# Optimization experiments

Hardware: AMD Instinct MI355X
Metric: run time of the kernel (lower is better)

The kernel has to match this reference:

```python
import jax, jax.numpy as jnp
import numpy as np

B, S, D_MODEL, D_HEAD = 8, 2048, 1024, 128
MAX_ROUNDS = 3
THRESH = 0.1
SCALE = 1.0 / np.sqrt(float(D_HEAD))


def setup_inputs() -> dict:
    key = jax.random.key(0)
    ks = jax.random.split(key, 12)

    def lin(k, out_d, in_d):
        # torch Linear weight layout [out, in], y = x @ W.T + b
        return (jax.random.normal(k, (out_d, in_d), jnp.float32) / np.sqrt(float(in_d))).astype(jnp.float32)

    thesis_w = lin(ks[3], D_HEAD, D_HEAD)
    return {
        "x": jax.random.normal(ks[0], (B, S, D_MODEL), jnp.float32),
        "wq": lin(ks[1], D_HEAD, D_MODEL),
        "wk": lin(ks[2], D_HEAD, D_MODEL),
        "wv": lin(ks[4], D_HEAD, D_MODEL),
        "thesis_w": thesis_w,  # antithesis weight is -thesis_w per __init__
        "thesis_b": 0.02 * jax.random.normal(ks[5], (D_HEAD,), jnp.float32),
        "anti_b": 0.02 * jax.random.normal(ks[6], (D_HEAD,), jnp.float32),
        "s_w1": lin(ks[7], D_HEAD, 3 * D_HEAD),
        "s_b1": jnp.zeros((D_HEAD,), jnp.float32),
        "s_w2": lin(ks[8], D_HEAD, D_HEAD),
        "s_b2": jnp.zeros((D_HEAD,), jnp.float32),
        "g_w": lin(ks[9], 1, 2 * D_HEAD),
        "g_b": jnp.zeros((1,), jnp.float32),
    }


def reference(x, wq, wk, wv, thesis_w, thesis_b, anti_b, s_w1, s_b1, s_w2, s_b2, g_w, g_b):
    # q/k/v projections (no bias)
    q = jnp.einsum("bsm,hm->bsh", x, wq)
    k = jnp.einsum("bsm,hm->bsh", x, wk)
    v = jnp.einsum("bsm,hm->bsh", x, wv)

    attn = jax.nn.softmax(jnp.einsum("bqh,bkh->bqk", q, k) * SCALE, axis=-1)
    # dropout is identity at eval time
    cur = jnp.einsum("bqk,bkh->bqh", attn, v)  # [B,S,Dh]

    # attn_weights and v never change across rounds, so thesis/antithesis are
    # round-invariant: compute the context projections once.
    context = cur
    thesis = context @ thesis_w.T + thesis_b
    anti = context @ (-thesis_w).T + anti_b  # antithesis weight = -thesis weight

    active = jnp.ones((B, S), dtype=bool)
    for _ in range(MAX_ROUNDS):
        # emulate `if not active_mask.any(): break` under jit
        any_active = jnp.any(active)
        am = active[..., None].astype(x.dtype)
        at, aa, ac = thesis * am, anti * am, cur * am

        h = jax.nn.relu(jnp.concatenate([at, aa, ac], axis=-1) @ s_w1.T + s_b1)
        synth = h @ s_w2.T + s_b2
        gate = jax.nn.sigmoid(jnp.concatenate([ac, synth], axis=-1) @ g_w.T + g_b)
        update = gate * (synth - ac) * 0.1
        new = cur + update  # applied to ALL tokens, matching original

        stable = jnp.linalg.norm(update, axis=-1) < THRESH  # new - cur == update
        cur = jnp.where(any_active, new, cur)
        active = jnp.where(any_active, active & ~stable, active)
    return cur
```

## Files before the change

### kernel.cpp

```cpp
#include <hip/hip_runtime.h>
#include <hip/hip_bf16.h>

#define B_   8
#define S_   2048
#define DM   1024
#define DH   128
#define BS_  16384
#define SCALE_  0.08838834764831845f
#define SCALE2_ 0.12751744f

typedef unsigned short u16;
typedef unsigned int   u32;
typedef _Float16 half8 __attribute__((ext_vector_type(8)));
typedef __bf16   bf16x8 __attribute__((ext_vector_type(8)));
typedef float    f32x4 __attribute__((ext_vector_type(4)));
typedef u32      u32x4 __attribute__((ext_vector_type(4)));

union H8 { u32x4 v; u32 u[4]; half8 h; bf16x8 b; };

__device__ __forceinline__ float bf2f(u16 u) {
    union { u32 i; float f; } w; w.i = ((u32)u) << 16; return w.f;
}
__device__ __forceinline__ void unpack8(uint4 v, float* f) {
    f[0] = bf2f(v.x & 0xffff); f[1] = bf2f(v.x >> 16);
// ... 208 lines not shown
                u32 w[4];
#pragma unroll
                for (int q = 0; q < 4; ++q)
                    w[q] = (u32)TS[key][d0 + 2 * q] | ((u32)TS[key][d0 + 2 * q + 1] << 16);
                kfrag[((size_t)(m0 / 16 + sub) * 4 + ks) * 64 + lf] = (u32x4){w[0], w[1], w[2], w[3]};
            }
        } else {
#pragma unroll
            for (int i = 0; i < 4; ++i) {
                const int f = tid + 256 * i;
                const int lf = f & 63, t = (f >> 6) & 7, sub = f >> 9;
                const int kb2 = sub * 32 + 8 * (lf >> 4);
                const int dh  = 16 * t + (lf & 15);
                u32 w[4];
#pragma unroll
                for (int q = 0; q < 4; ++q)
                    w[q] = (u32)TS[kb2 + 2 * q][dh] | ((u32)TS[kb2 + 2 * q + 1][dh] << 16);
                vfrag[((size_t)(m0 / 32 + sub) * 8 + t) * 64 + lf] = (u32x4){w[0], w[1], w[2], w[3]};
            }
        }
    }
}

template <bool WRITE_PARTIAL>
__device__ __forceinline__ void attn_body(
    const u32* qp, const u32x4* __restrict__ kfrag, const u32x4* __restrict__ vfrag,
    u16* outO, u16* outL, float* cur,
    int b, int q0, int kt0, int kt1, int part)
{
    const int tid = threadIdx.x;
    const int wave = tid >> 6, lane = tid & 63;
    const int qd = lane >> 4, c = lane & 15;

    __shared__ __align__(16) u16 PB[4][640];

    H8 Qh[4];
    {
        const u32* qr = qp + ((size_t)b * S_ + q0 + wave * 16 + c) * DH;
#pragma unroll
        for (int ks = 0; ks < 4; ++ks) {
            uint4 e0 = *(const uint4*)(qr + ks * 32 + qd * 8);
            uint4 e1 = *(const uint4*)(qr + ks * 32 + qd * 8 + 4);
            Qh[ks].u[0] = permHI(e0.y, e0.x); Qh[ks].u[1] = permHI(e0.w, e0.z);
            Qh[ks].u[2] = permHI(e1.y, e1.x); Qh[ks].u[3] = permHI(e1.w, e1.z);
        }
    }

    f32x4 O[8] = {};
    float lsum[4] = {};

    const u32x4* kb0 = kfrag + (size_t)b * 128 * 256;
    const u32x4* vb0 = vfrag + (size_t)b * 64 * 512;

    for (int kt = kt0; kt < kt1; ++kt) {
        const u32x4* kf = kb0 + (size_t)kt * 512;
        const u32x4* vf = vb0 + (size_t)kt * 512;

        f32x4 S0 = {}, S1 = {};
        __builtin_amdgcn_s_setprio(1);
#pragma unroll
        for (int ks = 0; ks < 4; ++ks) {
            H8 kh;
            kh.v = kf[ks * 64 + lane];
            S0 = __builtin_amdgcn_mfma_f32_16x16x32_f16(Qh[ks].h, kh.h, S0, 0, 0, 0);
            kh.v = kf[256 + ks * 64 + lane];
            S1 = __builtin_amdgcn_mfma_f32_16x16x32_f16(Qh[ks].h, kh.h, S1, 0, 0, 0);
        }
        __builtin_amdgcn_s_setprio(0);

        u16* pw = PB[wave];
#pragma unroll
        for (int r = 0; r < 4; ++r) {
            float e0 = exp2f(fmaf(S0[r], SCALE2_, -4.0f));
            float e1 = exp2f(fmaf(S1[r], SCALE2_, -4.0f));
            lsum[r] += e0 + e1;
            pw[(4 * qd + r) * 40 + c]      = f2h(e0);
            pw[(4 * qd + r) * 40 + 16 + c] = f2h(e1);
        }

        uint4 ev = *(const uint4*)&pw[c * 40 + 8 * qd];
        H8 Ph;
        Ph.u[0] = ev.x; Ph.u[1] = ev.y; Ph.u[2] = ev.z; Ph.u[3] = ev.w;

        __builtin_amdgcn_s_setprio(1);
#pragma unroll
        for (int t = 0; t < 8; ++t) {
            H8 vh;
            vh.v = vf[t * 64 + lane];
            O[t] = __builtin_amdgcn_mfma_f32_16x16x32_f16(Ph.h, vh.h, O[t], 0, 0, 0);
        }
        __builtin_amdgcn_s_setprio(0);
    }

    if (WRITE_PARTIAL) {
        float lred[4];
#pragma unroll
        for (int r = 0; r < 4; ++r) {
            float l = lsum[r];
            l += __shfl_xor(l, 1); l += __shfl_xor(l, 2);
            l += __shfl_xor(l, 4); l += __shfl_xor(l, 8);
            lred[r] = l;
        }
        const size_t rb = (size_t)b * S_ + q0 + wave * 16 + 4 * qd;
        u16* Op = outO + (size_t)part * ((size_t)BS_ * DH);
#pragma unroll
        for (int t = 0; t < 8; ++t)
#pragma unroll
            for (int r = 0; r < 4; ++r)
                Op[(rb + r) * DH + t * 16 + c] = f2h(O[t][r]);
        if (c == 0) {
            u16* lp = outL + (size_t)part * BS_;
#pragma unroll
            for (int r = 0; r < 4; ++r) lp[rb + r] = f2h(lred[r]);
        }
    } else {
        float linv[4];
#pragma unroll
        for (int r = 0; r < 4; ++r) {
            float l = lsum[r];
            l += __shfl_xor(l, 1); l += __shfl_xor(l, 2);
            l += __shfl_xor(l, 4); l += __shfl_xor(l, 8);
            linv[r] = 1.0f / l;
        }
        const size_t rb = (size_t)b * S_ + q0 + wave * 16 + 4 * qd;
#pragma unroll
        for (int t = 0; t < 8; ++t)
#pragma unroll
            for (int r = 0; r < 4; ++r)
                cur[(rb + r) * DH + t * 16 + c] = O[t][r] * linv[r];
    }
}

__global__ __launch_bounds__(256) void attn_kernel(
    const u32* qp, const u32x4* __restrict__ kfrag, const u32x4* __restrict__ vfrag, float* cur)
{
    const int rid = blockIdx.x + 32 * blockIdx.y;
    attn_body<false>(qp, kfrag, vfrag, nullptr, nullptr, cur,
                     rid & 7, ((rid >> 3) & 31) * 64, 0, S_ / 32, 0);
}

__global__ __launch_bounds__(256) void attn_split_kernel(
    const u32* qp, const u32x4* __restrict__ kfrag, const u32x4* __restrict__ vfrag,
    u16* __restrict__ Opart, u16* __restrict__ lpart)
{
    const int rid = blockIdx.x + 32 * (blockIdx.y + 8 * blockIdx.z);
    const int b    = rid & 7;
    const int qx   = (rid >> 3) & 31;
    const int part = rid >> 8;
    const int quart = S_ / 128;
    attn_body<true>(qp, kfrag, vfrag, Opart, lpart, nullptr,
                    b, qx * 64, part * quart, (part + 1) * quart, part);
}

__global__ __launch_bounds__(256) void combine_kernel(
    const u16* __restrict__ Opart, const u16* __restrict__ lpart,
    float* __restrict__ cur)
{
    const size_t N1 = (size_t)BS_ * DH;
    const size_t i0 = ((size_t)blockIdx.x * 256 + threadIdx.x) * 16;
    const int row = (int)(i0 >> 7);
    const float lt = h2f(lpart[row]) + h2f(lpart[BS_ + row])
                   + h2f(lpart[2 * BS_ + row]) + h2f(lpart[3 * BS_ + row]);
    const float linv = 1.0f / lt;
    float acc[16] = {};
#pragma unroll
    for (int p = 0; p < 4; ++p) {
        const u16* op = Opart + (size_t)p * N1 + i0;
        uint4 v0 = *(const uint4*)op;
        uint4 v1 = *(const uint4*)(op + 8);
        const u32 w[8] = {v0.x, v0.y, v0.z, v0.w, v1.x, v1.y, v1.z, v1.w};
#pragma unroll
        for (int j = 0; j < 8; ++j) {
            acc[2 * j]     += h2f((u16)(w[j] & 0xffff));
            acc[2 * j + 1] += h2f((u16)(w[j] >> 16));
        }
    }
#pragma unroll
    for (int t = 0; t < 4; ++t)
        *(float4*)(cur + i0 + t * 4) = make_float4(
            acc[4*t] * linv, acc[4*t+1] * linv, acc[4*t+2] * linv, acc[4*t+3] * linv);
}

__global__ __launch_bounds__(256) void prepack_rw_kernel(
    const void* __restrict__ tw, const void* __restrict__ w1, const void* __restrict__ w2,
    const int* __restrict__ flag, u32x4* __restrict__ pk)
{
    const int isb = *flag;
    const int gid = blockIdx.x * 256 + threadIdx.x;
    const int l = gid & 63, t = (gid >> 6) & 7, ks = (gid >> 9) & 3, mat = gid >> 11;
    const int row = 16 * t + (l & 15);
    const int k0  = ks * 32 + 8 * (l >> 4);
    float f[8];
    if (mat == 0)      ld8(tw, (size_t)row * DH + k0, isb, f);
    else if (mat <= 3) ld8(w1, (size_t)row * 384 + (mat - 1) * 128 + k0, isb, f);
    else               ld8(w2, (size_t)row * DH + k0, isb, f);
    u32x4 hi, lo;
    split8(f, hi, lo);
    const size_t base = (((size_t)mat * 4 + ks) * 16 + 2 * t) * 64 + l;
    pk[base] = hi; pk[base + 64] = lo;
}

struct Afrag { H8 h[4], l[4]; };
__device__ __forceinline__ void splitA(const float (&A)[4][8], Afrag& F) {
#pragma unroll
    for (int ks = 0; ks < 4; ++ks) split8(A[ks], F.h[ks].v, F.l[ks].v);
}

__global__ __launch_bounds__(256) void round_kernel(
    const float* cur0, const float* curr,
    const u32x4* __restrict__ pk, u16* __restrict__ T0,
    const void* __restrict__ tb, const void* __restrict__ ab,
    const void* __restrict__ b1, const void* __restrict__ b2,
    const void* __restrict__ gw, const void* __restrict__ gb,
    const int* __restrict__ flag, int* active, int* counts, int r,
    float* cur_out, void* dout)
{
    const int isb = *flag;
    const int tok0 = blockIdx.x * 16;
    const int tid = threadIdx.x;
    const bool last = (dout != nullptr);

    if (counts[r] <= 0) {
        if (last) {
            for (int e = tid; e < 16 * DH; e += 256) {
                size_t idx = (size_t)tok0 * DH + e;
                float v = curr[idx];
                if (isb) ((__hip_bfloat16*)dout)[idx] = __float2bfloat16(v);
                else     ((float*)dout)[idx] = v;
            }
        }
        return;
    }

    const int wave = tid >> 6, lane = tid & 63;
    const int qd = lane >> 4, c = lane & 15;

    __shared__ u32x4 WB[2][2][8][64];
    __shared__ u16 TS[16][132];
    __shared__ float actS[16], tbS[128], abS[128], b1S[128], b2S[128], gwS[256];
    __shared__ int blkcnt;

    auto stageBh = [&](int mat, int h) {
#pragma unroll
        for (int j = 0; j < 4; ++j) {
            const int g = wave * 4 + j, kl = g >> 3, t = g & 7;
            __builtin_amdgcn_global_load_lds(
                (const __attribute__((address_space(1))) u32*)(
                    pk + (((size_t)mat * 4 + 2 * h + kl) * 16 + 2 * t) * 64 + lane),
                (__attribute__((address_space(3))) u32*)&WB[h][kl][t][0],
                16, 0, 0);
        }
    };
    auto gemmBh = [&](const Afrag& F, int h, f32x4 (&acc)[2]) {
#pragma unroll
        for (int kl = 0; kl < 2; ++kl) {
            const int ks = 2 * h + kl;
#pragma unroll
            for (int tl = 0; tl < 2; ++tl) {
                H8 bh; bh.v = WB[h][kl][2 * wave + tl][lane];
                acc[tl] = __builtin_amdgcn_mfma_f32_16x16x32_f16(F.l[ks].h, bh.h, acc[tl], 0, 0, 0);
                acc[tl] = __builtin_amdgcn_mfma_f32_16x16x32_f16(F.h[ks].h, bh.h, acc[tl], 0, 0, 0);
            }
        }
    };
    auto stageFq = [&](int mat, int q, int buf) {
#pragma unroll
        for (int j = 0; j < 4; ++j) {
            const int g = wave * 4 + j, p = g & 1, t = g >> 1;
            __builtin_amdgcn_global_load_lds(
                (const __attribute__((address_space(1))) u32*)(
                    pk + (((size_t)mat * 4 + q) * 16 + 2 * t + p) * 64 + lane),
                (__attribute__((address_space(3))) u32*)&WB[buf][p][t][0],
                16, 0, 0);
        }
    };
    auto gemmFq = [&](const Afrag& F, int q, int buf, f32x4 (&acc)[2]) {
#pragma unroll
        for (int tl = 0; tl < 2; ++tl) {
            H8 bh, bl;
            bh.v = WB[buf][0][2 * wave + tl][lane];
            bl.v = WB[buf][1][2 * wave + tl][lane];
            acc[tl] = __builtin_amdgcn_mfma_f32_16x16x32_f16(F.l[q].h, bh.h, acc[tl], 0, 0, 0);
            acc[tl] = __builtin_amdgcn_mfma_f32_16x16x32_f16(F.h[q].h, bl.h, acc[tl], 0, 0, 0);
            acc[tl] = __builtin_amdgcn_mfma_f32_16x16x32_f16(F.h[q].h, bh.h, acc[tl], 0, 0, 0);
        }
    };
    auto GEMMF = [&](int mat, const Afrag& F, f32x4 (&acc)[2]) {
        for (int q = 0; q < 4; ++q) {
            stageFq(mat, q, q & 1);
            __syncthreads();
            gemmFq(F, q, q & 1, acc);
            __syncthreads();
        }
    };

    const int hr = 4 * qd;
    const int rowl = c;

    auto writeTS = [&](const f32x4 (&acc)[2], const float* bias, bool relu) {
#pragma unroll
        for (int tl = 0; tl < 2; ++tl)
#pragma unroll
            for (int rr = 0; rr < 4; ++rr) {
                const int col = 16 * (2 * wave + tl) + c;
                float v = acc[tl][rr] + (bias ? bias[col] : 0.0f);
                TS[hr + rr][col] = f2h(relu ? fmaxf(v, 0.0f) : v);
            }
    };
    auto buildAt = [&](Afrag& F, float am_r) {
        float Ac[4][8];
#pragma unroll
        for (int ks = 0; ks < 4; ++ks)
#pragma unroll
            for (int j = 0; j < 8; ++j) {
                const int k = ks * 32 + 8 * qd + j;
                Ac[ks][j] = (h2f(TS[rowl][k]) + tbS[k]) * am_r;
            }
        splitA(Ac, F);
    };
    auto buildAa = [&](Afrag& F, float am_r) {
        float Ac[4][8];
#pragma unroll
        for (int ks = 0; ks < 4; ++ks)
#pragma unroll
            for (int j = 0; j < 8; ++j) {
                const int k = ks * 32 + 8 * qd + j;
                Ac[ks][j] = (abS[k] - h2f(TS[rowl][k])) * am_r;
            }
        splitA(Ac, F);
    };
    auto buildAc = [&](Afrag& F, float am_r) {
        float Ac[4][8];
        const float* cr = curr + (size_t)(tok0 + rowl) * DH;
#pragma unroll
        for (int ks = 0; ks < 4; ++ks) {
            float4 a0 = *(const float4*)(cr + ks * 32 + 8 * qd);
            float4 a1 = *(const float4*)(cr + ks * 32 + 8 * qd + 4);
            Ac[ks][0] = a0.x * am_r; Ac[ks][1] = a0.y * am_r;
            Ac[ks][2] = a0.z * am_r; Ac[ks][3] = a0.w * am_r;
            Ac[ks][4] = a1.x * am_r; Ac[ks][5] = a1.y * am_r;
            Ac[ks][6] = a1.z * am_r; Ac[ks][7] = a1.w * am_r;
        }
        splitA(Ac, F);
    };
    auto buildAh = [&](Afrag& F) {
        float Ac[4][8];
#pragma unroll
        for (int ks = 0; ks < 4; ++ks)
#pragma unroll
            for (int j = 0; j < 8; ++j)
                Ac[ks][j] = h2f(TS[rowl][ks * 32 + 8 * qd + j]);
        splitA(Ac, F);
    };

    if (tid < 16) actS[tid] = active[tok0 + tid] ? 1.0f : 0.0f;
    if (tid < 128) {
        tbS[tid] = ldE(tb, tid, isb); abS[tid] = ldE(ab, tid, isb);
        b1S[tid] = ldE(b1, tid, isb); b2S[tid] = ldE(b2, tid, isb);
    }
    gwS[tid] = ldE(gw, tid, isb);
    if (tid == 0) blkcnt = 0;
    const float gbf = ldE(gb, 0, isb);

    if (isb) {
        f32x4 acc1[2] = {};
        if (r == 0) {
            float A1[4][8];
            const float* cr = cur0 + (size_t)(tok0 + rowl) * DH;
#pragma unroll
            for (int ks = 0; ks < 4; ++ks) {
                *(float4*)&A1[ks][0] = *(const float4*)(cr + ks * 32 + 8 * qd);
                *(float4*)&A1[ks][4] = *(const float4*)(cr + ks * 32 + 8 * qd + 4);
            }
            Afrag FA; splitA(A1, FA);
            stageBh(0, 0);
            __syncthreads();
            stageBh(0, 1);
            f32x4 accT[2] = {};
            gemmBh(FA, 0, accT);
            __syncthreads();
            stageBh(1, 0);
            gemmBh(FA, 1, accT);
            writeTS(accT, nullptr, false);
            __syncthreads();
            for (int i = tid; i < 16 * 64; i += 256) {
                const int row = i >> 6, c2 = (i & 63) * 2;
                *(u32*)&T0[(size_t)(tok0 + row) * DH + c2] = *(const u32*)&TS[row][c2];
            }
        } else {
            stageBh(1, 0);
            for (int i = tid; i < 16 * 64; i += 256) {
                const int row = i >> 6, c2 = (i & 63) * 2;
                *(u32*)&TS[row][c2] = *(const u32*)&T0[(size_t)(tok0 + row) * DH + c2];
            }
            __syncthreads();
        }
        const float am_r = actS[rowl];
        {
            Afrag FC; buildAt(FC, am_r);
            stageBh(1, 1);
            gemmBh(FC, 0, acc1);
            __syncthreads();
            stageBh(2, 0);
            gemmBh(FC, 1, acc1);
            __syncthreads();
        }
        {
            Afrag FC; buildAa(FC, am_r);
            stageBh(2, 1);
            gemmBh(FC, 0, acc1);
            __syncthreads();
            stageBh(3, 0);
            gemmBh(FC, 1, acc1);
            __syncthreads();
        }
        {
            Afrag FC; buildAc(FC, am_r);
            stageBh(3, 1);
            gemmBh(FC, 0, acc1);
            __syncthreads();
            stageBh(4, 0);
            gemmBh(FC, 1, acc1);
        }
        writeTS(acc1, b1S, true);
        __syncthreads();
        {
            Afrag FC; buildAh(FC);
            stageBh(4, 1);
            f32x4 acc2[2] = {};
            gemmBh(FC, 0, acc2);
            __syncthreads();
            gemmBh(FC, 1, acc2);
            writeTS(acc2, b2S, false);
        }
        __syncthreads();
    } else {
        __syncthreads();
        f32x4 acc1[2] = {};
        if (r == 0) {
            float A1[4][8];
            const float* cr = cur0 + (size_t)(tok0 + rowl) * DH;
#pragma unroll
            for (int ks = 0; ks < 4; ++ks) {
                *(float4*)&A1[ks][0] = *(const float4*)(cr + ks * 32 + 8 * qd);
                *(float4*)&A1[ks][4] = *(const float4*)(cr + ks * 32 + 8 * qd + 4);
            }
            Afrag FA; splitA(A1, FA);
            f32x4 accT[2] = {};
            GEMMF(0, FA, accT);
            writeTS(accT, nullptr, false);
            __syncthreads();
            for (int i = tid; i < 16 * 64; i += 256) {
                const int row = i >> 6, c2 = (i & 63) * 2;
                *(u32*)&T0[(size_t)(tok0 + row) * DH + c2] = *(const u32*)&TS[row][c2];
            }
        } else {
            for (int i = tid; i < 16 * 64; i += 256) {
                const int row = i >> 6, c2 = (i & 63) * 2;
                *(u32*)&TS[row][c2] = *(const u32*)&T0[(size_t)(tok0 + row) * DH + c2];
            }
            __syncthreads();
        }
        const float am_r = actS[rowl];
        { Afrag FC; buildAt(FC, am_r); GEMMF(1, FC, acc1); }
        { Afrag FC; buildAa(FC, am_r); GEMMF(2, FC, acc1); }
        { Afrag FC; buildAc(FC, am_r); GEMMF(3, FC, acc1); }
        writeTS(acc1, b1S, true);
        __syncthreads();
        {
            Afrag FC; buildAh(FC);
            f32x4 acc2[2] = {};
            GEMMF(4, FC, acc2);
            writeTS(acc2, b2S, false);
        }
        __syncthreads();
    }

    const int tok = tid >> 4, d0 = (tid & 15) * 8;
    const float am = actS[tok];
    const float* cp = curr + (size_t)(tok0 + tok) * DH + d0;
    float cv[8];
    {
        float4 v0 = *(const float4*)cp;
        float4 v1 = *(const float4*)(cp + 4);
        cv[0] = v0.x; cv[1] = v0.y; cv[2] = v0.z; cv[3] = v0.w;
        cv[4] = v1.x; cv[5] = v1.y; cv[6] = v1.z; cv[7] = v1.w;
    }
    float srow[8];
#pragma unroll
    for (int e = 0; e < 8; ++e) srow[e] = h2f(TS[tok][d0 + e]);
    float gp = 0.0f;
#pragma unroll
    for (int e = 0; e < 8; ++e)
        gp += cv[e] * am * gwS[d0 + e] + srow[e] * gwS[128 + d0 + e];
    gp += __shfl_xor(gp, 1, 16);
    gp += __shfl_xor(gp, 2, 16);
    gp += __shfl_xor(gp, 4, 16);
    gp += __shfl_xor(gp, 8, 16);
    const float gate = 1.0f / (1.0f + __expf(-(gp + gbf)));
    float ss = 0.0f; float up[8];
#pragma unroll
    for (int e = 0; e < 8; ++e) {
        float u = gate * (srow[e] - cv[e] * am) * 0.1f;
        up[e] = u; ss += u * u;
    }
    ss += __shfl_xor(ss, 1, 16);
    ss += __shfl_xor(ss, 2, 16);
    ss += __shfl_xor(ss, 4, 16);
    ss += __shfl_xor(ss, 8, 16);
    const bool stable = sqrtf(ss) < 0.1f;

    if (last) {
        size_t off = (size_t)(tok0 + tok) * DH + d0;
        if (isb) {
            __hip_bfloat16* op = (__hip_bfloat16*)dout + off;
#pragma unroll
            for (int e = 0; e < 8; ++e) op[e] = __float2bfloat16(cv[e] + up[e]);
        } else {
            float* op = (float*)dout + off;
            *(float4*)op       = make_float4(cv[0] + up[0], cv[1] + up[1], cv[2] + up[2], cv[3] + up[3]);
            *(float4*)(op + 4) = make_float4(cv[4] + up[4], cv[5] + up[5], cv[6] + up[6], cv[7] + up[7]);
        }
    } else {
        float* op = cur_out + (size_t)(tok0 + tok) * DH + d0;
        *(float4*)op       = make_float4(cv[0] + up[0], cv[1] + up[1], cv[2] + up[2], cv[3] + up[3]);
        *(float4*)(op + 4) = make_float4(cv[4] + up[4], cv[5] + up[5], cv[6] + up[6], cv[7] + up[7]);
    }
    const int newact = (am > 0.0f && !stable) ? 1 : 0;
    if ((tid & 15) == 0) {
        active[tok0 + tok] = newact;
        if (newact) atomicAdd(&blkcnt, 1);
    }
    __syncthreads();
    if (tid == 0 && blkcnt > 0) atomicAdd(&counts[r + 1], blkcnt);
}

extern "C" void kernel_launch(void* const* d_in, const int* in_sizes, int n_in,
                              void* d_out, int out_size, void* d_ws, size_t ws_size,
                              hipStream_t stream) {
    const void* x  = d_in[0];
    const void* wq = d_in[1];
    const void* wk = d_in[2];
    const void* wv = d_in[3];
    const void* tw = d_in[4];
    const void* tb = d_in[5];
    const void* ab = d_in[6];
    const void* w1 = d_in[7];
    const void* b1 = d_in[8];
    const void* w2 = d_in[9];
    const void* b2 = d_in[10];
    const void* gw = d_in[11];
    const void* gb = d_in[12];

    u32* ws = (u32*)d_ws;
    const size_t N1 = (size_t)BS_ * DH;
    u32* qp = ws;
    u32* kp = ws + N1;
    u32* vp = ws + 2 * N1;
    int* active = (int*)(ws + 3 * N1);
    int* counts = active + BS_;
    int* flag   = counts + 4;
    float* cur0  = (float*)qp;
    float* cur_r = (float*)kp;
    u16* Opart16 = (u16*)(ws + 3 * N1 + 32768);
    u16* lpart16 = (u16*)(ws + 5 * N1 + 32768);
    const bool big_ws = ws_size >= (size_t)42300000;
    u32x4* wpk = (u32x4*)(ws + 3 * N1 + 32768);
    u32x4* pkRW = (u32x4*)vp;
    u16*   T0c  = (u16*)(vp + 131072);
    u32x4* kfragP = (u32x4*)kp;
    u32x4* vfragP = (u32x4*)vp;

    init_kernel<<<dim3(BS_ / 256), 256, 0, stream>>>(x, flag, active, counts);
    prepack_w_kernel<<<dim3(192), 256, 0, stream>>>(wq, wk, wv, flag, wpk);
    qkv_kernel<<<dim3(BS_ / 64, 1, 3), 256, 0, stream>>>(x, wpk, flag, qp, kfragP, vfragP);
    if (big_ws) {
        attn_split_kernel<<<dim3(S_ / 64, B_, 4), 256, 0, stream>>>(qp, kfragP, vfragP, Opart16, lpart16);
        combine_kernel<<<dim3(512), 256, 0, stream>>>(Opart16, lpart16, cur0);
    } else {
        attn_kernel<<<dim3(S_ / 64, B_), 256, 0, stream>>>(qp, kfragP, vfragP, cur0);
    }
    prepack_rw_kernel<<<dim3(40), 256, 0, stream>>>(tw, w1, w2, flag, pkRW);
    round_kernel<<<dim3(BS_ / 16), 256, 0, stream>>>(
        cur0, cur0, pkRW, T0c, tb, ab, b1, b2, gw, gb, flag, active, counts, 0, cur_r, nullptr);
    round_kernel<<<dim3(BS_ / 16), 256, 0, stream>>>(
        cur0, cur_r, pkRW, T0c, tb, ab, b1, b2, gw, gb, flag, active, counts, 1, cur_r, nullptr);
    round_kernel<<<dim3(BS_ / 16), 256, 0, stream>>>(
        cur0, cur_r, pkRW, T0c, tb, ab, b1, b2, gw, gb, flag, active, counts, 2, cur_r, d_out);
}
```

Baseline: 255.9 us.

## Fuse split-attention combine into specialized round-0 kernel; widen later rounds to 32 tokens

The separate combine kernel is removed. Its reduction of the four attention partials is folded into a new round0 kernel that builds the first-round context in shared memory and skips the active-mask multiply, since every token starts active. Rounds 1 and 2 now process 32 tokens per block with a 2x2 wave layout, which halves the number of weight-staging passes per token and lets the weight tiles be staged whole into a larger LDS buffer. This saves a launch and a full fp32 round trip of the context, at the cost of more LDS and registers per block in the later rounds.

```diff
diff --git a/kernel.cpp b/kernel.cpp
--- a/kernel.cpp
+++ b/kernel.cpp
@@ -384,35 +384,6 @@
                     b, qx * 64, part * quart, (part + 1) * quart, part);
 }
 
-__global__ __launch_bounds__(256) void combine_kernel(
-    const u16* __restrict__ Opart, const u16* __restrict__ lpart,
-    float* __restrict__ cur)
-{
-    const size_t N1 = (size_t)BS_ * DH;
-    const size_t i0 = ((size_t)blockIdx.x * 256 + threadIdx.x) * 16;
-    const int row = (int)(i0 >> 7);
-    const float lt = h2f(lpart[row]) + h2f(lpart[BS_ + row])
-                   + h2f(lpart[2 * BS_ + row]) + h2f(lpart[3 * BS_ + row]);
-    const float linv = 1.0f / lt;
-    float acc[16] = {};
-#pragma unroll
-    for (int p = 0; p < 4; ++p) {
-        const u16* op = Opart + (size_t)p * N1 + i0;
-        uint4 v0 = *(const uint4*)op;
-        uint4 v1 = *(const uint4*)(op + 8);
-        const u32 w[8] = {v0.x, v0.y, v0.z, v0.w, v1.x, v1.y, v1.z, v1.w};
-#pragma unroll
-        for (int j = 0; j < 8; ++j) {
-            acc[2 * j]     += h2f((u16)(w[j] & 0xffff));
-            acc[2 * j + 1] += h2f((u16)(w[j] >> 16));
-        }
-    }
-#pragma unroll
-    for (int t = 0; t < 4; ++t)
-        *(float4*)(cur + i0 + t * 4) = make_float4(
-            acc[4*t] * linv, acc[4*t+1] * linv, acc[4*t+2] * linv, acc[4*t+3] * linv);
-}
-
 __global__ __launch_bounds__(256) void prepack_rw_kernel(
     const void* __restrict__ tw, const void* __restrict__ w1, const void* __restrict__ w2,
     const int* __restrict__ flag, u32x4* __restrict__ pk)
@@ -438,9 +409,301 @@
     for (int ks = 0; ks < 4; ++ks) split8(A[ks], F.h[ks].v, F.l[ks].v);
 }
 
+__global__ __launch_bounds__(256) void round0_kernel(
+    const float* __restrict__ cur0g,
+    const u16* __restrict__ Opart, const u16* __restrict__ lpart,
+    const u32x4* __restrict__ pk, u16* __restrict__ T0,
+    const void* __restrict__ tb, const void* __restrict__ ab,
+    const void* __restrict__ b1, const void* __restrict__ b2,
+    const void* __restrict__ gw, const void* __restrict__ gb,
+    const int* __restrict__ flag, int* active, int* counts,
+    float* cur_out, int combine)
+{
+    const int isb = *flag;
+    const int tok0 = blockIdx.x * 16;
+    const int tid = threadIdx.x;
+    const int wave = tid >> 6, lane = tid & 63;
+    const int qd = lane >> 4, c = lane & 15;
+
+    __shared__ u32x4 WB[2][2][8][64];
+    __shared__ u16 TS[16][132];
+    __shared__ float CS[16][128];
+    __shared__ float tbS[128], abS[128], b1S[128], b2S[128], gwS[256];
+    __shared__ int blkcnt;
+
+    auto stageBh = [&](int mat, int h) {
+#pragma unroll
+        for (int j = 0; j < 4; ++j) {
+            const int g = wave * 4 + j, kl = g >> 3, t = g & 7;
+            __builtin_amdgcn_global_load_lds(
+                (const __attribute__((address_space(1))) u32*)(
+                    pk + (((size_t)mat * 4 + 2 * h + kl) * 16 + 2 * t) * 64 + lane),
+                (__attribute__((address_space(3))) u32*)&WB[h][kl][t][0],
+                16, 0, 0);
+        }
+    };
+    auto gemmBh = [&](const Afrag& F, int h, f32x4 (&acc)[2]) {
+#pragma unroll
+        for (int kl = 0; kl < 2; ++kl) {
+            const int ks = 2 * h + kl;
+#pragma unroll
+            for (int tl = 0; tl < 2; ++tl) {
+                H8 bh; bh.v = WB[h][kl][2 * wave + tl][lane];
+                acc[tl] = __builtin_amdgcn_mfma_f32_16x16x32_f16(F.l[ks].h, bh.h, acc[tl], 0, 0, 0);
+                acc[tl] = __builtin_amdgcn_mfma_f32_16x16x32_f16(F.h[ks].h, bh.h, acc[tl], 0, 0, 0);
+            }
+        }
+    };
+    auto stageFq = [&](int mat, int q, int buf) {
+#pragma unroll
+        for (int j = 0; j < 4; ++j) {
+            const int g = wave * 4 + j, p = g & 1, t = g >> 1;
+            __builtin_amdgcn_global_load_lds(
+                (const __attribute__((address_space(1))) u32*)(
+                    pk + (((size_t)mat * 4 + q) * 16 + 2 * t + p) * 64 + lane),
+                (__attribute__((address_space(3))) u32*)&WB[buf][p][t][0],
+                16, 0, 0);
+        }
+    };
+    auto gemmFq = [&](const Afrag& F, int q, int buf, f32x4 (&acc)[2]) {
+#pragma unroll
+        for (int tl = 0; tl < 2; ++tl) {
+            H8 bh, bl;
+            bh.v = WB[buf][0][2 * wave + tl][lane];
+            bl.v = WB[buf][1][2 * wave + tl][lane];
+            acc[tl] = __builtin_amdgcn_mfma_f32_16x16x32_f16(F.l[q].h, bh.h, acc[tl], 0, 0, 0);
+            acc[tl] = __builtin_amdgcn_mfma_f32_16x16x32_f16(F.h[q].h, bl.h, acc[tl], 0, 0, 0);
+            acc[tl] = __builtin_amdgcn_mfma_f32_16x16x32_f16(F.h[q].h, bh.h, acc[tl], 0, 0, 0);
+        }
+    };
+    auto GEMMF = [&](int mat, const Afrag& F, f32x4 (&acc)[2]) {
+        for (int q = 0; q < 4; ++q) {
+            stageFq(mat, q, q & 1);
+            __syncthreads();
+            gemmFq(F, q, q & 1, acc);
+            __syncthreads();
+        }
+    };
+
+    const int hr = 4 * qd;
+    const int rowl = c;
+
+    auto writeTS = [&](const f32x4 (&acc)[2], const float* bias, bool relu) {
+#pragma unroll
+        for (int tl = 0; tl < 2; ++tl)
+#pragma unroll
+            for (int rr = 0; rr < 4; ++rr) {
+                const int col = 16 * (2 * wave + tl) + c;
+                float v = acc[tl][rr] + (bias ? bias[col] : 0.0f);
+                TS[hr + rr][col] = f2h(relu ? fmaxf(v, 0.0f) : v);
+            }
+    };
+    auto buildA1 = [&](Afrag& F) {
+        float Ac[4][8];
+#pragma unroll
+        for (int ks = 0; ks < 4; ++ks)
+#pragma unroll
+            for (int j = 0; j < 8; ++j)
+                Ac[ks][j] = CS[rowl][ks * 32 + 8 * qd + j];
+        splitA(Ac, F);
+    };
+    auto buildAt = [&](Afrag& F) {
+        float Ac[4][8];
+#pragma unroll
+        for (int ks = 0; ks < 4; ++ks)
+#pragma unroll
+            for (int j = 0; j < 8; ++j) {
+                const int k = ks * 32 + 8 * qd + j;
+                Ac[ks][j] = h2f(TS[rowl][k]) + tbS[k];
+            }
+        splitA(Ac, F);
+    };
+    auto buildAa = [&](Afrag& F) {
+        float Ac[4][8];
+#pragma unroll
+        for (int ks = 0; ks < 4; ++ks)
+#pragma unroll
+            for (int j = 0; j < 8; ++j) {
+                const int k = ks * 32 + 8 * qd + j;
+                Ac[ks][j] = abS[k] - h2f(TS[rowl][k]);
+            }
+        splitA(Ac, F);
+    };
+    auto buildAh = [&](Afrag& F) {
+        float Ac[4][8];
+#pragma unroll
+        for (int ks = 0; ks < 4; ++ks)
+#pragma unroll
+            for (int j = 0; j < 8; ++j)
+                Ac[ks][j] = h2f(TS[rowl][ks * 32 + 8 * qd + j]);
+        splitA(Ac, F);
+    };
+
+    if (tid < 128) {
+        tbS[tid] = ldE(tb, tid, isb); abS[tid] = ldE(ab, tid, isb);
+        b1S[tid] = ldE(b1, tid, isb); b2S[tid] = ldE(b2, tid, isb);
+    }
+    gwS[tid] = ldE(gw, tid, isb);
+    if (tid == 0) blkcnt = 0;
+    const float gbf = ldE(gb, 0, isb);
+    {
+        const int row = tid >> 4, d0 = (tid & 15) * 8;
+        float a8[8];
+        if (combine) {
+            const size_t grow = (size_t)(tok0 + row);
+            const float lt = h2f(lpart[grow]) + h2f(lpart[BS_ + grow])
+                           + h2f(lpart[2 * BS_ + grow]) + h2f(lpart[3 * BS_ + grow]);
+            const float linv = 1.0f / lt;
+            float acc[8] = {};
+            const size_t N1 = (size_t)BS_ * DH;
+#pragma unroll
+            for (int p = 0; p < 4; ++p) {
+                const u16* op = Opart + (size_t)p * N1 + grow * DH + d0;
+                uint4 v0 = *(const uint4*)op;
+                const u32 w[4] = {v0.x, v0.y, v0.z, v0.w};
+#pragma unroll
+                for (int j = 0; j < 4; ++j) {
+                    acc[2 * j]     += h2f((u16)(w[j] & 0xffff));
+                    acc[2 * j + 1] += h2f((u16)(w[j] >> 16));
+                }
+            }
+#pragma unroll
+            for (int e = 0; e < 8; ++e) a8[e] = acc[e] * linv;
+        } else {
+            const float* cr = cur0g + (size_t)(tok0 + row) * DH + d0;
+            float4 v0 = *(const float4*)cr;
+            float4 v1 = *(const float4*)(cr + 4);
+            a8[0] = v0.x; a8[1] = v0.y; a8[2] = v0.z; a8[3] = v0.w;
+            a8[4] = v1.x; a8[5] = v1.y; a8[6] = v1.z; a8[7] = v1.w;
+        }
+#pragma unroll
+        for (int e = 0; e < 8; ++e) CS[row][d0 + e] = a8[e];
+    }
+
+    if (isb) {
+        stageBh(0, 0);
+        __syncthreads();
+        Afrag FA; buildA1(FA);
+        stageBh(0, 1);
+        f32x4 accT[2] = {};
+        gemmBh(FA, 0, accT);
+        __syncthreads();
+        stageBh(1, 0);
+        gemmBh(FA, 1, accT);
+        writeTS(accT, nullptr, false);
+        __syncthreads();
+        for (int i = tid; i < 16 * 64; i += 256) {
+            const int row = i >> 6, c2 = (i & 63) * 2;
+            *(u32*)&T0[(size_t)(tok0 + row) * DH + c2] = *(const u32*)&TS[row][c2];
+        }
+        f32x4 acc1[2] = {};
+        {
+            Afrag FC; buildAt(FC);
+            stageBh(1, 1);
+            gemmBh(FC, 0, acc1);
+            __syncthreads();
+            stageBh(2, 0);
+            gemmBh(FC, 1, acc1);
+            __syncthreads();
+        }
+        {
+            Afrag FC; buildAa(FC);
+            stageBh(2, 1);
+            gemmBh(FC, 0, acc1);
+            __syncthreads();
+            stageBh(3, 0);
+            gemmBh(FC, 1, acc1);
+            __syncthreads();
+        }
+        {
+            Afrag FC; buildA1(FC);
+            stageBh(3, 1);
+            gemmBh(FC, 0, acc1);
+            __syncthreads();
+            stageBh(4, 0);
+            gemmBh(FC, 1, acc1);
+        }
+        writeTS(acc1, b1S, true);
+        __syncthreads();
+        {
+            Afrag FC; buildAh(FC);
+            stageBh(4, 1);
+            f32x4 acc2[2] = {};
+            gemmBh(FC, 0, acc2);
+            __syncthreads();
+            gemmBh(FC, 1, acc2);
+            writeTS(acc2, b2S, false);
+        }
+        __syncthreads();
+    } else {
+        __syncthreads();
+        Afrag FA; buildA1(FA);
+        f32x4 accT[2] = {};
+        GEMMF(0, FA, accT);
+        writeTS(accT, nullptr, false);
+        __syncthreads();
+        for (int i = tid; i < 16 * 64; i += 256) {
+            const int row = i >> 6, c2 = (i & 63) * 2;
+            *(u32*)&T0[(size_t)(tok0 + row) * DH + c2] = *(const u32*)&TS[row][c2];
+        }
+        f32x4 acc1[2] = {};
+        { Afrag FC; buildAt(FC); GEMMF(1, FC, acc1); }
+        { Afrag FC; buildAa(FC); GEMMF(2, FC, acc1); }
+        { Afrag FC; buildA1(FC); GEMMF(3, FC, acc1); }
+        writeTS(acc1, b1S, true);
+        __syncthreads();
+        {
+            Afrag FC; buildAh(FC);
+            f32x4 acc2[2] = {};
+            GEMMF(4, FC, acc2);
+            writeTS(acc2, b2S, false);
+        }
+        __syncthreads();
+    }
+
+    const int tok = tid >> 4, d0g = (tid & 15) * 8;
+    float cv[8];
+#pragma unroll
+    for (int e = 0; e < 8; ++e) cv[e] = CS[tok][d0g + e];
+    float srow[8];
+#pragma unroll
+    for (int e = 0; e < 8; ++e) srow[e] = h2f(TS[tok][d0g + e]);
+    float gp = 0.0f;
+#pragma unroll
+    for (int e = 0; e < 8; ++e)
+        gp += cv[e] * gwS[d0g + e] + srow[e] * gwS[128 + d0g + e];
+    gp += __shfl_xor(gp, 1, 16);
+    gp += __shfl_xor(gp, 2, 16);
+    gp += __shfl_xor(gp, 4, 16);
+    gp += __shfl_xor(gp, 8, 16);
+    const float gate = 1.0f / (1.0f + __expf(-(gp + gbf)));
+    float ss = 0.0f; float up[8];
+#pragma unroll
+    for (int e = 0; e < 8; ++e) {
+        float u = gate * (srow[e] - cv[e]) * 0.1f;
+        up[e] = u; ss += u * u;
+    }
+    ss += __shfl_xor(ss, 1, 16);
+    ss += __shfl_xor(ss, 2, 16);
+    ss += __shfl_xor(ss, 4, 16);
+    ss += __shfl_xor(ss, 8, 16);
+    const bool stable = sqrtf(ss) < 0.1f;
+
+    float* op = cur_out + (size_t)(tok0 + tok) * DH + d0g;
+    *(float4*)op       = make_float4(cv[0] + up[0], cv[1] + up[1], cv[2] + up[2], cv[3] + up[3]);
+    *(float4*)(op + 4) = make_float4(cv[4] + up[4], cv[5] + up[5], cv[6] + up[6], cv[7] + up[7]);
+    const int newact = stable ? 0 : 1;
+    if ((tid & 15) == 0) {
+        active[tok0 + tok] = newact;
+        if (newact) atomicAdd(&blkcnt, 1);
+    }
+    __syncthreads();
+    if (tid == 0 && blkcnt > 0) atomicAdd(&counts[1], blkcnt);
+}
+
 __global__ __launch_bounds__(256) void round_kernel(
-    const float* cur0, const float* curr,
-    const u32x4* __restrict__ pk, u16* __restrict__ T0,
+    const float* curr,
+    const u32x4* __restrict__ pk, const u16* __restrict__ T0,
     const void* __restrict__ tb, const void* __restrict__ ab,
     const void* __restrict__ b1, const void* __restrict__ b2,
     const void* __restrict__ gw, const void* __restrict__ gb,
@@ -448,13 +711,13 @@
     float* cur_out, void* dout)
 {
     const int isb = *flag;
-    const int tok0 = blockIdx.x * 16;
+    const int tok0 = blockIdx.x * 32;
     const int tid = threadIdx.x;
     const bool last = (dout != nullptr);
 
     if (counts[r] <= 0) {
         if (last) {
-            for (int e = tid; e < 16 * DH; e += 256) {
+            for (int e = tid; e < 32 * DH; e += 256) {
                 size_t idx = (size_t)tok0 * DH + e;
                 float v = curr[idx];
                 if (isb) ((__hip_bfloat16*)dout)[idx] = __float2bfloat16(v);
@@ -466,80 +729,96 @@
 
     const int wave = tid >> 6, lane = tid & 63;
     const int qd = lane >> 4, c = lane & 15;
-
-    __shared__ u32x4 WB[2][2][8][64];
-    __shared__ u16 TS[16][132];
-    __shared__ float actS[16], tbS[128], abS[128], b1S[128], b2S[128], gwS[256];
+    const int rowg = wave >> 1, colh = wave & 1;
+
+    __shared__ u32x4 WB[2][4][8][64];
+    __shared__ u16 TS[32][132];
+    __shared__ float actS[32], tbS[128], abS[128], b1S[128], b2S[128], gwS[256];
     __shared__ int blkcnt;
 
-    auto stageBh = [&](int mat, int h) {
-#pragma unroll
-        for (int j = 0; j < 4; ++j) {
-            const int g = wave * 4 + j, kl = g >> 3, t = g & 7;
+    auto stageB = [&](int mat, int buf) {
+#pragma unroll
+        for (int j = 0; j < 8; ++j) {
+            const int g = wave * 8 + j, ks = g >> 3, t = g & 7;
             __builtin_amdgcn_global_load_lds(
                 (const __attribute__((address_space(1))) u32*)(
-                    pk + (((size_t)mat * 4 + 2 * h + kl) * 16 + 2 * t) * 64 + lane),
-                (__attribute__((address_space(3))) u32*)&WB[h][kl][t][0],
+                    pk + (((size_t)mat * 4 + ks) * 16 + 2 * t) * 64 + lane),
+                (__attribute__((address_space(3))) u32*)&WB[buf][ks][t][0],
                 16, 0, 0);
         }
     };
-    auto gemmBh = [&](const Afrag& F, int h, f32x4 (&acc)[2]) {
+    auto stageF = [&](int mat, int h, int buf) {
+#pragma unroll
+        for (int j = 0; j < 8; ++j) {
+            const int g = wave * 8 + j, kl = g >> 4, p = (g >> 3) & 1, t = g & 7;
+            __builtin_amdgcn_global_load_lds(
+                (const __attribute__((address_space(1))) u32*)(
+                    pk + (((size_t)mat * 4 + 2 * h + kl) * 16 + 2 * t + p) * 64 + lane),
+                (__attribute__((address_space(3))) u32*)&WB[buf][kl * 2 + p][t][0],
+                16, 0, 0);
+        }
+    };
+    auto gemmB = [&](const Afrag& F, int buf, f32x4 (&acc)[4]) {
+#pragma unroll
+        for (int ks = 0; ks < 4; ++ks)
+#pragma unroll
+            for (int tl = 0; tl < 4; ++tl) {
+                H8 bh; bh.v = WB[buf][ks][4 * colh + tl][lane];
+                acc[tl] = __builtin_amdgcn_mfma_f32_16x16x32_f16(F.l[ks].h, bh.h, acc[tl], 0, 0, 0);
+                acc[tl] = __builtin_amdgcn_mfma_f32_16x16x32_f16(F.h[ks].h, bh.h, acc[tl], 0, 0, 0);
+            }
+    };
+    auto gemmFh = [&](const Afrag& F, int h, int buf, f32x4 (&acc)[4]) {
 #pragma unroll
         for (int kl = 0; kl < 2; ++kl) {
             const int ks = 2 * h + kl;
 #pragma unroll
-            for (int tl = 0; tl < 2; ++tl) {
-                H8 bh; bh.v = WB[h][kl][2 * wave + tl][lane];
+            for (int tl = 0; tl < 4; ++tl) {
+                H8 bh, bl;
+                bh.v = WB[buf][kl * 2][4 * colh + tl][lane];
+                bl.v = WB[buf][kl * 2 + 1][4 * colh + tl][lane];
                 acc[tl] = __builtin_amdgcn_mfma_f32_16x16x32_f16(F.l[ks].h, bh.h, acc[tl], 0, 0, 0);
+                acc[tl] = __builtin_amdgcn_mfma_f32_16x16x32_f16(F.h[ks].h, bl.h, acc[tl], 0, 0, 0);
                 acc[tl] = __builtin_amdgcn_mfma_f32_16x16x32_f16(F.h[ks].h, bh.h, acc[tl], 0, 0, 0);
             }
         }
     };
-    auto stageFq = [&](int mat, int q, int buf) {
-#pragma unroll
-        for (int j = 0; j < 4; ++j) {
-            const int g = wave * 4 + j, p = g & 1, t = g >> 1;
-            __builtin_amdgcn_global_load_lds(
-                (const __attribute__((address_space(1))) u32*)(
-                    pk + (((size_t)mat * 4 + q) * 16 + 2 * t + p) * 64 + lane),
-                (__attribute__((address_space(3))) u32*)&WB[buf][p][t][0],
-                16, 0, 0);
-        }
-    };
-    auto gemmFq = [&](const Afrag& F, int q, int buf, f32x4 (&acc)[2]) {
-#pragma unroll
-        for (int tl = 0; tl < 2; ++tl) {
-            H8 bh, bl;
-            bh.v = WB[buf][0][2 * wave + tl][lane];
-            bl.v = WB[buf][1][2 * wave + tl][lane];
-            acc[tl] = __builtin_amdgcn_mfma_f32_16x16x32_f16(F.l[q].h, bh.h, acc[tl], 0, 0, 0);
-            acc[tl] = __builtin_amdgcn_mfma_f32_16x16x32_f16(F.h[q].h, bl.h, acc[tl], 0, 0, 0);
-            acc[tl] = __builtin_amdgcn_mfma_f32_16x16x32_f16(F.h[q].h, bh.h, acc[tl], 0, 0, 0);
-        }
-    };
-    auto GEMMF = [&](int mat, const Afrag& F, f32x4 (&acc)[2]) {
-        for (int q = 0; q < 4; ++q) {
-            stageFq(mat, q, q & 1);
-            __syncthreads();
-            gemmFq(F, q, q & 1, acc);
-            __syncthreads();
-        }
-    };
-
-    const int hr = 4 * qd;
-    const int rowl = c;
-
-    auto writeTS = [&](const f32x4 (&acc)[2], const float* bias, bool relu) {
-#pragma unroll
-        for (int tl = 0; tl < 2; ++tl)
-#pragma unroll
-            for (int rr = 0; rr < 4; ++rr) {
-                const int col = 16 * (2 * wave + tl) + c;
-                float v = acc[tl][rr] + (bias ? bias[col] : 0.0f);
-                TS[hr + rr][col] = f2h(relu ? fmaxf(v, 0.0f) : v);
-            }
-    };
-    auto buildAt = [&](Afrag& F, float am_r) {
+    auto STAGE = [&](int mat, int buf) { if (isb) stageB(mat, buf); else stageF(mat, 0, buf); };
+    auto GEMM = [&](int mat, const Afrag& F, int buf, f32x4 (&acc)[4]) {
+        if (isb) {
+            gemmB(F, buf, acc);
+        } else {
+            gemmFh(F, 0, buf, acc);
+            __syncthreads();
+            stageF(mat, 1, buf);
+            __syncthreads();
+            gemmFh(F, 1, buf, acc);
+        }
+    };
+
+    STAGE(1, 1);
+    if (tid < 32) actS[tid] = active[tok0 + tid] ? 1.0f : 0.0f;
+    if (tid < 128) {
+        tbS[tid] = ldE(tb, tid, isb); abS[tid] = ldE(ab, tid, isb);
+        b1S[tid] = ldE(b1, tid, isb); b2S[tid] = ldE(b2, tid, isb);
+    }
+    gwS[tid] = ldE(gw, tid, isb);
+    if (tid == 0) blkcnt = 0;
+    const float gbf = ldE(gb, 0, isb);
+
+    const int rowl = 16 * rowg + c;
+    const int hr   = 16 * rowg + 4 * qd;
+
+    for (int i = tid; i < 32 * 64; i += 256) {
+        const int row = i >> 6, c2 = (i & 63) * 2;
+        *(u32*)&TS[row][c2] = *(const u32*)&T0[(size_t)(tok0 + row) * DH + c2];
+    }
+    __syncthreads();
+
+    STAGE(2, 0);
+    f32x4 acc1[4] = {};
+    const float am_r = actS[rowl];
+    {
         float Ac[4][8];
 #pragma unroll
         for (int ks = 0; ks < 4; ++ks)
@@ -548,9 +827,13 @@
                 const int k = ks * 32 + 8 * qd + j;
                 Ac[ks][j] = (h2f(TS[rowl][k]) + tbS[k]) * am_r;
             }
-        splitA(Ac, F);
-    };
-    auto buildAa = [&](Afrag& F, float am_r) {
+        Afrag FC; splitA(Ac, FC);
+        GEMM(1, FC, 1, acc1);
+    }
+    __syncthreads();
+
+    STAGE(3, 1);
+    {
         float Ac[4][8];
 #pragma unroll
         for (int ks = 0; ks < 4; ++ks)
@@ -559,9 +842,13 @@
                 const int k = ks * 32 + 8 * qd + j;
                 Ac[ks][j] = (abS[k] - h2f(TS[rowl][k])) * am_r;
             }
-        splitA(Ac, F);
-    };
-    auto buildAc = [&](Afrag& F, float am_r) {
+        Afrag FC; splitA(Ac, FC);
+        GEMM(2, FC, 0, acc1);
+    }
+    __syncthreads();
+
+    STAGE(4, 0);
+    {
         float Ac[4][8];
         const float* cr = curr + (size_t)(tok0 + rowl) * DH;
 #pragma unroll
@@ -573,173 +860,68 @@
             Ac[ks][4] = a1.x * am_r; Ac[ks][5] = a1.y * am_r;
             Ac[ks][6] = a1.z * am_r; Ac[ks][7] = a1.w * am_r;
         }
-        splitA(Ac, F);
-    };
-    auto buildAh = [&](Afrag& F) {
+        Afrag FC; splitA(Ac, FC);
+        GEMM(3, FC, 1, acc1);
+    }
+#pragma unroll
+    for (int tl = 0; tl < 4; ++tl)
+#pragma unroll
+        for (int rr = 0; rr < 4; ++rr) {
+            const int col = 16 * (4 * colh + tl) + c;
+            TS[hr + rr][col] = f2h(fmaxf(acc1[tl][rr] + b1S[col], 0.0f));
+        }
+    __syncthreads();
+
+    {
         float Ac[4][8];
 #pragma unroll
         for (int ks = 0; ks < 4; ++ks)
 #pragma unroll
             for (int j = 0; j < 8; ++j)
                 Ac[ks][j] = h2f(TS[rowl][ks * 32 + 8 * qd + j]);
-        splitA(Ac, F);
-    };
-
-    if (tid < 16) actS[tid] = active[tok0 + tid] ? 1.0f : 0.0f;
-    if (tid < 128) {
-        tbS[tid] = ldE(tb, tid, isb); abS[tid] = ldE(ab, tid, isb);
-        b1S[tid] = ldE(b1, tid, isb); b2S[tid] = ldE(b2, tid, isb);
-    }
-    gwS[tid] = ldE(gw, tid, isb);
-    if (tid == 0) blkcnt = 0;
-    const float gbf = ldE(gb, 0, isb);
-
-    if (isb) {
-        f32x4 acc1[2] = {};
-        if (r == 0) {
-            float A1[4][8];
-            const float* cr = cur0 + (size_t)(tok0 + rowl) * DH;
-#pragma unroll
-            for (int ks = 0; ks < 4; ++ks) {
-                *(float4*)&A1[ks][0] = *(const float4*)(cr + ks * 32 + 8 * qd);
-                *(float4*)&A1[ks][4] = *(const float4*)(cr + ks * 32 + 8 * qd + 4);
-            }
-            Afrag FA; splitA(A1, FA);
-            stageBh(0, 0);
-            __syncthreads();
-            stageBh(0, 1);
-            f32x4 accT[2] = {};
-            gemmBh(FA, 0, accT);
-            __syncthreads();
-            stageBh(1, 0);
-            gemmBh(FA, 1, accT);
-            writeTS(accT, nullptr, false);
-            __syncthreads();
-            for (int i = tid; i < 16 * 64; i += 256) {
-                const int row = i >> 6, c2 = (i & 63) * 2;
-                *(u32*)&T0[(size_t)(tok0 + row) * DH + c2] = *(const u32*)&TS[row][c2];
-            }
-        } else {
-            stageBh(1, 0);
-            for (int i = tid; i < 16 * 64; i += 256) {
-                const int row = i >> 6, c2 = (i & 63) * 2;
-                *(u32*)&TS[row][c2] = *(const u32*)&T0[(size_t)(tok0 + row) * DH + c2];
-            }
-            __syncthreads();
-        }
-        const float am_r = actS[rowl];
-        {
-            Afrag FC; buildAt(FC, am_r);
-            stageBh(1, 1);
-            gemmBh(FC, 0, acc1);
-            __syncthreads();
-            stageBh(2, 0);
-            gemmBh(FC, 1, acc1);
-            __syncthreads();
-        }
-        {
-            Afrag FC; buildAa(FC, am_r);
-            stageBh(2, 1);
-            gemmBh(FC, 0, acc1);
-            __syncthreads();
-            stageBh(3, 0);
-            gemmBh(FC, 1, acc1);
-            __syncthreads();
-        }
-        {
-            Afrag FC; buildAc(FC, am_r);
-            stageBh(3, 1);
-            gemmBh(FC, 0, acc1);
-            __syncthreads();
-            stageBh(4, 0);
-            gemmBh(FC, 1, acc1);
-        }
-        writeTS(acc1, b1S, true);
-        __syncthreads();
-        {
-            Afrag FC; buildAh(FC);
-            stageBh(4, 1);
-            f32x4 acc2[2] = {};
-            gemmBh(FC, 0, acc2);
-            __syncthreads();
-            gemmBh(FC, 1, acc2);
-            writeTS(acc2, b2S, false);
-        }
-        __syncthreads();
-    } else {
-        __syncthreads();
-        f32x4 acc1[2] = {};
-        if (r == 0) {
-            float A1[4][8];
-            const float* cr = cur0 + (size_t)(tok0 + rowl) * DH;
-#pragma unroll
-            for (int ks = 0; ks < 4; ++ks) {
-                *(float4*)&A1[ks][0] = *(const float4*)(cr + ks * 32 + 8 * qd);
-                *(float4*)&A1[ks][4] = *(const float4*)(cr + ks * 32 + 8 * qd + 4);
-            }
-            Afrag FA; splitA(A1, FA);
-            f32x4 accT[2] = {};
-            GEMMF(0, FA, accT);
-            writeTS(accT, nullptr, false);
-            __syncthreads();
-            for (int i = tid; i < 16 * 64; i += 256) {
-                const int row = i >> 6, c2 = (i & 63) * 2;
-                *(u32*)&T0[(size_t)(tok0 + row) * DH + c2] = *(const u32*)&TS[row][c2];
-            }
-        } else {
-            for (int i = tid; i < 16 * 64; i += 256) {
-                const int row = i >> 6, c2 = (i & 63) * 2;
-                *(u32*)&TS[row][c2] = *(const u32*)&T0[(size_t)(tok0 + row) * DH + c2];
-            }
-            __syncthreads();
-        }
-        const float am_r = actS[rowl];
-        { Afrag FC; buildAt(FC, am_r); GEMMF(1, FC, acc1); }
-        { Afrag FC; buildAa(FC, am_r); GEMMF(2, FC, acc1); }
-        { Afrag FC; buildAc(FC, am_r); GEMMF(3, FC, acc1); }
-        writeTS(acc1, b1S, true);
-        __syncthreads();
-        {
-            Afrag FC; buildAh(FC);
-            f32x4 acc2[2] = {};
-            GEMMF(4, FC, acc2);
-            writeTS(acc2, b2S, false);
-        }
-        __syncthreads();
-    }
-
-    const int tok = tid >> 4, d0 = (tid & 15) * 8;
+        Afrag FC; splitA(Ac, FC);
+        f32x4 acc2[4] = {};
+        GEMM(4, FC, 0, acc2);
+        __syncthreads();
+#pragma unroll
+        for (int tl = 0; tl < 4; ++tl)
+#pragma unroll
+            for (int rr = 0; rr < 4; ++rr) {
+                const int col = 16 * (4 * colh + tl) + c;
+                TS[hr + rr][col] = f2h(acc2[tl][rr] + b2S[col]);
+            }
+    }
+    __syncthreads();
+
+    const int tok = tid >> 3, d0 = (tid & 7) * 16;
     const float am = actS[tok];
     const float* cp = curr + (size_t)(tok0 + tok) * DH + d0;
-    float cv[8];
-    {
-        float4 v0 = *(const float4*)cp;
-        float4 v1 = *(const float4*)(cp + 4);
-        cv[0] = v0.x; cv[1] = v0.y; cv[2] = v0.z; cv[3] = v0.w;
-        cv[4] = v1.x; cv[5] = v1.y; cv[6] = v1.z; cv[7] = v1.w;
-    }
-    float srow[8];
-#pragma unroll
-    for (int e = 0; e < 8; ++e) srow[e] = h2f(TS[tok][d0 + e]);
+    float cv[16];
+#pragma unroll
+    for (int t = 0; t < 4; ++t) {
+        float4 vv = *(const float4*)(cp + t * 4);
+        cv[t * 4] = vv.x; cv[t * 4 + 1] = vv.y; cv[t * 4 + 2] = vv.z; cv[t * 4 + 3] = vv.w;
+    }
+    float srow[16];
+#pragma unroll
+    for (int e = 0; e < 16; ++e) srow[e] = h2f(TS[tok][d0 + e]);
     float gp = 0.0f;
 #pragma unroll
-    for (int e = 0; e < 8; ++e)
+    for (int e = 0; e < 16; ++e)
         gp += cv[e] * am * gwS[d0 + e] + srow[e] * gwS[128 + d0 + e];
-    gp += __shfl_xor(gp, 1, 16);
-    gp += __shfl_xor(gp, 2, 16);
-    gp += __shfl_xor(gp, 4, 16);
-    gp += __shfl_xor(gp, 8, 16);
+    gp += __shfl_xor(gp, 1, 8);
+    gp += __shfl_xor(gp, 2, 8);
+    gp += __shfl_xor(gp, 4, 8);
     const float gate = 1.0f / (1.0f + __expf(-(gp + gbf)));
-    float ss = 0.0f; float up[8];
-#pragma unroll
-    for (int e = 0; e < 8; ++e) {
+    float ss = 0.0f; float up[16];
+#pragma unroll
+    for (int e = 0; e < 16; ++e) {
         float u = gate * (srow[e] - cv[e] * am) * 0.1f;
         up[e] = u; ss += u * u;
     }
-    ss += __shfl_xor(ss, 1, 16);
-    ss += __shfl_xor(ss, 2, 16);
-    ss += __shfl_xor(ss, 4, 16);
-    ss += __shfl_xor(ss, 8, 16);
+    ss += __shfl_xor(ss, 1, 8);
+    ss += __shfl_xor(ss, 2, 8);
+    ss += __shfl_xor(ss, 4, 8);
     const bool stable = sqrtf(ss) < 0.1f;
 
     if (last) {
@@ -747,19 +929,23 @@
         if (isb) {
             __hip_bfloat16* op = (__hip_bfloat16*)dout + off;
 #pragma unroll
-            for (int e = 0; e < 8; ++e) op[e] = __float2bfloat16(cv[e] + up[e]);
+            for (int e = 0; e < 16; ++e) op[e] = __float2bfloat16(cv[e] + up[e]);
         } else {
             float* op = (float*)dout + off;
-            *(float4*)op       = make_float4(cv[0] + up[0], cv[1] + up[1], cv[2] + up[2], cv[3] + up[3]);
-            *(float4*)(op + 4) = make_float4(cv[4] + up[4], cv[5] + up[5], cv[6] + up[6], cv[7] + up[7]);
+#pragma unroll
+            for (int t = 0; t < 4; ++t)
+                *(float4*)(op + t * 4) = make_float4(cv[t * 4] + up[t * 4], cv[t * 4 + 1] + up[t * 4 + 1],
+                                                     cv[t * 4 + 2] + up[t * 4 + 2], cv[t * 4 + 3] + up[t * 4 + 3]);
         }
     } else {
         float* op = cur_out + (size_t)(tok0 + tok) * DH + d0;
-        *(float4*)op       = make_float4(cv[0] + up[0], cv[1] + up[1], cv[2] + up[2], cv[3] + up[3]);
-        *(float4*)(op + 4) = make_float4(cv[4] + up[4], cv[5] + up[5], cv[6] + up[6], cv[7] + up[7]);
+#pragma unroll
+        for (int t = 0; t < 4; ++t)
+            *(float4*)(op + t * 4) = make_float4(cv[t * 4] + up[t * 4], cv[t * 4 + 1] + up[t * 4 + 1],
+                                                 cv[t * 4 + 2] + up[t * 4 + 2], cv[t * 4 + 3] + up[t * 4 + 3]);
     }
     const int newact = (am > 0.0f && !stable) ? 1 : 0;
-    if ((tid & 15) == 0) {
+    if ((tid & 7) == 0) {
         active[tok0 + tok] = newact;
         if (newact) atomicAdd(&blkcnt, 1);
     }
@@ -808,15 +994,15 @@
     qkv_kernel<<<dim3(BS_ / 64, 1, 3), 256, 0, stream>>>(x, wpk, flag, qp, kfragP, vfragP);
     if (big_ws) {
         attn_split_kernel<<<dim3(S_ / 64, B_, 4), 256, 0, stream>>>(qp, kfragP, vfragP, Opart16, lpart16);
-        combine_kernel<<<dim3(512), 256, 0, stream>>>(Opart16, lpart16, cur0);
     } else {
         attn_kernel<<<dim3(S_ / 64, B_), 256, 0, stream>>>(qp, kfragP, vfragP, cur0);
     }
     prepack_rw_kernel<<<dim3(40), 256, 0, stream>>>(tw, w1, w2, flag, pkRW);
-    round_kernel<<<dim3(BS_ / 16), 256, 0, stream>>>(
-        cur0, cur0, pkRW, T0c, tb, ab, b1, b2, gw, gb, flag, active, counts, 0, cur_r, nullptr);
-    round_kernel<<<dim3(BS_ / 16), 256, 0, stream>>>(
-        cur0, cur_r, pkRW, T0c, tb, ab, b1, b2, gw, gb, flag, active, counts, 1, cur_r, nullptr);
-    round_kernel<<<dim3(BS_ / 16), 256, 0, stream>>>(
-        cur0, cur_r, pkRW, T0c, tb, ab, b1, b2, gw, gb, flag, active, counts, 2, cur_r, d_out);
-}
+    round0_kernel<<<dim3(BS_ / 16), 256, 0, stream>>>(
+        cur0, Opart16, lpart16, pkRW, T0c, tb, ab, b1, b2, gw, gb,
+        flag, active, counts, cur_r, big_ws ? 1 : 0);
+    round_kernel<<<dim3(BS_ / 32), 256, 0, stream>>>(
+        cur_r, pkRW, T0c, tb, ab, b1, b2, gw, gb, flag, active, counts, 1, cur_r, nullptr);
+    round_kernel<<<dim3(BS_ / 32), 256, 0, stream>>>(
+        cur_r, pkRW, T0c, tb, ab, b1, b2, gw, gb, flag, active, counts, 2, cur_r, d_out);
+}
```

Result: no change. 253.2 us (median of 2 runs) (-1.1%).
